# Kernel tuning notes

Measured on AMD Instinct MI355X. Metric: run time of the kernel, lower is better.

Reference implementation:

```python
import jax, jax.numpy as jnp
import numpy as np

B, L, D, K = 8, 1024, 1024, 128
VOCAB, N_ATOM_FEAT, N_TIMESTEPS = 160, 512, 1000
NEG = jnp.finfo(jnp.float32).min
SCALING = K ** (-0.5)


def setup_inputs() -> dict:
    key = jax.random.key(0)
    ks = jax.random.split(key, 14)
    inp = {}
    # forward args
    inp["token_id"] = jax.random.randint(ks[0], (B, L), 0, VOCAB)  # 0 => padding
    inp["node_attr"] = jax.random.randint(ks[1], (B, L, 9), 0, N_ATOM_FEAT)
    inp["is_molecule"] = jax.random.randint(ks[2], (B,), 0, 2).astype(bool)
    inp["pos"] = jax.random.normal(ks[3], (B, L, 3), jnp.float32) * 10.0
    inp["time_step"] = jax.random.randint(ks[4], (B, L), 0, N_TIMESTEPS)
    # learned parameters
    inp["embed_table"] = jax.random.normal(ks[5], (VOCAB, D), jnp.float32) * 0.02
    inp["atom_feat_table"] = jax.random.normal(ks[6], (N_ATOM_FEAT, D), jnp.float32) * 0.02
    inp["time_table"] = jax.random.normal(ks[7], (N_TIMESTEPS, D), jnp.float32) * 0.02
    inp["time_w1"] = jax.random.normal(ks[8], (D, D), jnp.float32) * (D ** -0.5)
    inp["time_b1"] = jnp.zeros((D,), jnp.float32)
    inp["time_w2"] = jax.random.normal(ks[9], (D, D), jnp.float32) * (D ** -0.5)
    inp["time_b2"] = jnp.zeros((D,), jnp.float32)
    inp["pos_emb_w"] = jax.random.normal(ks[10], (1, K), jnp.float32)          # Linear(1 -> K), no bias
    inp["pos_feature_w"] = jax.random.normal(ks[11], (K, D), jnp.float32) * (K ** -0.5)  # Linear(K -> D), no bias
    return inp


def _pos_emb(pos, padding_mask, pos_emb_w, pos_feature_w):
    # pos: [B,L,3], padding_mask: [B,L] bool
    delta = pos[:, :, None, :] - pos[:, None, :, :]          # [B,L,L,3]
    dist = 1.0 / (jnp.linalg.norm(delta, axis=-1) + 1.0)     # [B,L,L]
    # masked_fill on key side (expand_mask) and query side (padding_mask)
    mask = padding_mask[:, None, :] | padding_mask[:, :, None]
    dist = jnp.where(mask, NEG, dist)
    # value projection: Linear(1->K) on per-atom radial norm, zeroed at padding
    pe = jnp.linalg.norm(pos, axis=-1, keepdims=True) @ pos_emb_w  # [B,L,K]
    pe = jnp.where(padding_mask[:, :, None], 0.0, pe)
    attn = jax.nn.softmax(dist * SCALING, axis=-1)            # [B,L,L]
    pfe = jnp.einsum("bqk,bkc->bqc", attn, pe)                 # [B,L,K]
    pfe = pfe @ pos_feature_w                                  # [B,L,D]
    return jnp.where(padding_mask[:, :, None], 0.0, pfe)


def reference(token_id, node_attr, is_molecule, pos, time_step,
              embed_table, atom_feat_table, time_table,
              time_w1, time_b1, time_w2, time_b2,
              pos_emb_w, pos_feature_w):
    padding_mask = token_id == 0                               # [B,L]
    x = embed_table[token_id]                                  # [B,L,D]
    # 2D atom features: embed cols 1: and sum over feature axis
    atom_emb = atom_feat_table[node_attr[:, :, 1:]].sum(axis=-2)  # [B,L,D]
    atom_emb = jnp.where(is_molecule[:, None, None], atom_emb, 0.0)
    x = x + atom_emb
    # time step encoder: learnable embedding + Linear-SiLU-Linear MLP
    t = time_table[time_step]                                   # [B,L,D]
    time_embed = jax.nn.silu(t @ time_w1 + time_b1) @ time_w2 + time_b2
    x = x + time_embed
    # pairwise 3D positional embedding (softmax attention over 1/(r+1))
    x = x + _pos_emb(pos, padding_mask, pos_emb_w, pos_feature_w)
    return x, padding_mask
```

## Files before the change

kernel.cpp:

```cpp
#include <hip/hip_runtime.h>
#include <hip/hip_bf16.h>
#include <math.h>

#define BB 8
#define LL 1024
#define DD 1024
#define KK 128
#define NTS 1000
#define VOCAB 160
#define NATOM 512
#define SCALE 0.08838834764831845f

typedef __attribute__((ext_vector_type(8))) short short8;
typedef __attribute__((ext_vector_type(4))) float f32x4;

__device__ __forceinline__ unsigned short f2bf(float x) {
    __hip_bfloat16 h = __float2bfloat16(x);
    return *reinterpret_cast<unsigned short*>(&h);
}
__device__ __forceinline__ float bf2f(unsigned short u) {
    return __uint_as_float(((unsigned int)u) << 16);
}

__global__ __launch_bounds__(256) void prep_kernel(
    const float* __restrict__ w1,
    const float* __restrict__ w2,
    const float* __restrict__ embed_f,
    const float* __restrict__ atom_f,
    const float* __restrict__ pos_emb_w,
    const float* __restrict__ pos_feature_w,
    const void*  __restrict__ is_mol_raw,
    unsigned short* __restrict__ W1t,
    unsigned short* __restrict__ W2t,
    unsigned short* __restrict__ embed_bf,
    unsigned short* __restrict__ atom_bf,
    float* __restrict__ v,
    int*   __restrict__ is_mol_out)
{
    __shared__ float tile[32][33];
    const int blk = blockIdx.x;

    if (blk < 2048) {
        const int which = blk >> 10;
        const int idx = blk & 1023;
        const float* in = which ? w2 : w1;
        unsigned short* out = which ? W2t : W1t;
        const int bx = (idx & 31) * 32, by = (idx >> 5) * 32;
        const int tx = threadIdx.x & 31, ty = threadIdx.x >> 5;
        #pragma unroll
        for (int r = 0; r < 32; r += 8)
            tile[ty + r][tx] = in[(size_t)(by + ty + r) * DD + bx + tx];
        __syncthreads();
        #pragma unroll
        for (int r = 0; r < 32; r += 8)
            out[(size_t)(bx + ty + r) * DD + by + tx] = f2bf(tile[tx][ty + r]);
    } else if (blk < 2208) {
        const int e = ((blk - 2048) * 256 + threadIdx.x) * 4;
        float4 vv = *(const float4*)&embed_f[e];
        ushort4 o = { f2bf(vv.x), f2bf(vv.y), f2bf(vv.z), f2bf(vv.w) };
        *(ushort4*)&embed_bf[e] = o;
    } else if (blk < 2720) {
        const int e = ((blk - 2208) * 256 + threadIdx.x) * 4;
        float4 vv = *(const float4*)&atom_f[e];
        ushort4 o = { f2bf(vv.x), f2bf(vv.y), f2bf(vv.z), f2bf(vv.w) };
        *(ushort4*)&atom_bf[e] = o;
    } else if (blk < 2724) {
        int d = (blk - 2720) * 256 + threadIdx.x;
        float acc = 0.0f;
        #pragma unroll 4
        for (int c = 0; c < KK; ++c)
            acc += pos_emb_w[c] * pos_feature_w[c * DD + d];
        v[d] = acc;
    } else {
        if (threadIdx.x == 0) {
            const int* ip = (const int*)is_mol_raw;
            const unsigned char* cp = (const unsigned char*)is_mol_raw;
            bool all_bin = true;
            for (int i = 0; i < BB; ++i) {
                int x = ip[i];
                if (x != 0 && x != 1) all_bin = false;
            }
            for (int i = 0; i < BB; ++i)
                is_mol_out[i] = all_bin ? (ip[i] != 0) : (cp[i] != 0);
        }
    }
}

template <int MODE>
__global__ __launch_bounds__(256) void mfma_gemm32(
    const void* __restrict__ Ap,
    const unsigned short* __restrict__ Bt,
    const float* __restrict__ bias,
    unsigned short* __restrict__ Cout)
{
    __shared__ __align__(16) unsigned short As[32][136];
    __shared__ __align__(16) unsigned short Bs[32][136];

    const int tid  = threadIdx.x;
    const int lane = tid & 63;
    const int wave = tid >> 6;
    const int wm = wave >> 1, wn = wave & 1;
    const int quad = lane >> 4, l16 = lane & 15;
    const int mBase = blockIdx.y * 32, nBase = blockIdx.x * 32;

    f32x4 acc = {0.f, 0.f, 0.f, 0.f};

    const int r0 = tid >> 4, ko = (tid & 15) * 8;
    const int rowB0 = nBase + r0,      rowB1 = nBase + r0 + 16;
    int rowA0 = mBase + r0,            rowA1 = mBase + r0 + 16;
    if (MODE == 0) {
        if (rowA0 >= NTS) rowA0 = NTS - 1;
        if (rowA1 >= NTS) rowA1 = NTS - 1;
    }

    for (int k0 = 0; k0 < DD; k0 += 128) {
        if (MODE == 0) {
            const float* A = (const float*)Ap;
            float4 a00 = *(const float4*)&A[(size_t)rowA0 * DD + k0 + ko];
            float4 a01 = *(const float4*)&A[(size_t)rowA0 * DD + k0 + ko + 4];
            float4 a10 = *(const float4*)&A[(size_t)rowA1 * DD + k0 + ko];
            float4 a11 = *(const float4*)&A[(size_t)rowA1 * DD + k0 + ko + 4];
            short8 s0, s1;
            s0[0]=f2bf(a00.x); s0[1]=f2bf(a00.y); s0[2]=f2bf(a00.z); s0[3]=f2bf(a00.w);
            s0[4]=f2bf(a01.x); s0[5]=f2bf(a01.y); s0[6]=f2bf(a01.z); s0[7]=f2bf(a01.w);
            s1[0]=f2bf(a10.x); s1[1]=f2bf(a10.y); s1[2]=f2bf(a10.z); s1[3]=f2bf(a10.w);
            s1[4]=f2bf(a11.x); s1[5]=f2bf(a11.y); s1[6]=f2bf(a11.z); s1[7]=f2bf(a11.w);
            *(short8*)&As[r0][ko]      = s0;
            *(short8*)&As[r0 + 16][ko] = s1;
        } else {
            const unsigned short* A = (const unsigned short*)Ap;
            float4 a0 = *(const float4*)&A[(size_t)rowA0 * DD + k0 + ko];
            float4 a1 = *(const float4*)&A[(size_t)rowA1 * DD + k0 + ko];
            *(float4*)&As[r0][ko]      = a0;
            *(float4*)&As[r0 + 16][ko] = a1;
        }
        float4 b0 = *(const float4*)&Bt[(size_t)rowB0 * DD + k0 + ko];
        float4 b1 = *(const float4*)&Bt[(size_t)rowB1 * DD + k0 + ko];
        *(float4*)&Bs[r0][ko]      = b0;
        *(float4*)&Bs[r0 + 16][ko] = b1;
        __syncthreads();

        #pragma unroll
        for (int kk = 0; kk < 128; kk += 32) {
            short8 af = *(const short8*)&As[wm * 16 + l16][kk + quad * 8];
            short8 bf = *(const short8*)&Bs[wn * 16 + l16][kk + quad * 8];
            acc = __builtin_amdgcn_mfma_f32_16x16x32_bf16(af, bf, acc, 0, 0, 0);
        }
        __syncthreads();
    }

    const int col = nBase + wn * 16 + l16;
    const float bv = bias[col];
    #pragma unroll
    for (int r4 = 0; r4 < 4; ++r4) {
        const int row = mBase + wm * 16 + quad * 4 + r4;
        float val = acc[r4] + bv;
        if (MODE == 0) val = val / (1.0f + __expf(-val));
        Cout[(size_t)row * DD + col] = f2bf(val);
    }
}

__global__ __launch_bounds__(256) void fused_all(
    const int*   __restrict__ token_id,
    const int*   __restrict__ node_attr,
    const float* __restrict__ pos,
    const int*   __restrict__ time_step,
    const unsigned short* __restrict__ embed_bf,
    const unsigned short* __restrict__ atom_bf,
    const unsigned short* __restrict__ Ebf,
    const float* __restrict__ v,
    const int*   __restrict__ is_mol,
    float* __restrict__ out)
{
    __shared__ float4 keys[LL];
    __shared__ float  sS[8];

    const int blk   = blockIdx.x;
    const int batch = blk >> 7;
    const int q0    = (blk & 127) << 3;
    const int tid   = threadIdx.x;
    const int lane  = tid & 63, wave = tid >> 6;

    #pragma unroll
    for (int i = 0; i < 4; ++i) {
        const int k = tid + i * 256;
        const int t = batch * LL + k;
        const float x = pos[t * 3 + 0];
        const float y = pos[t * 3 + 1];
        const float z = pos[t * 3 + 2];
        const int tok = token_id[t];
        const float n = sqrtf(x * x + y * y + z * z);
        keys[k] = make_float4(x, y, z, tok == 0 ? -1.0f : n);
    }
    __syncthreads();

    #pragma unroll
    for (int qi = 0; qi < 2; ++qi) {
        const int ql = wave * 2 + qi;
        const float4 qk = keys[q0 + ql];
        float lsum = 0.0f, lws = 0.0f;
        #pragma unroll 4
        for (int i = 0; i < 16; ++i) {
            const float4 kd = keys[lane + i * 64];
            const float dx = qk.x - kd.x, dy = qk.y - kd.y, dz = qk.z - kd.z;
            const float dn = sqrtf(dx * dx + dy * dy + dz * dz);
            const float e = __expf(SCALE / (dn + 1.0f));
            const bool valid = kd.w >= 0.0f;
            const float ev = valid ? e : 0.0f;
            lsum += ev;
            lws  += ev * (valid ? kd.w : 0.0f);
        }
        #pragma unroll
        for (int off = 32; off > 0; off >>= 1) {
            lsum += __shfl_xor(lsum, off);
            lws  += __shfl_xor(lws,  off);
        }
        if (lane == 0)
            sS[ql] = (qk.w < 0.0f) ? 0.0f : (lws / lsum);
    }
    __syncthreads();

    const int im   = is_mol[batch];
    const int half = tid >> 7;
    const int tl   = tid & 127;
    const int j    = tl * 8;
    const float4 v0 = *(const float4*)&v[j];
    const float4 v1 = *(const float4*)&v[j + 4];

    #pragma unroll
    for (int qp = 0; qp < 4; ++qp) {
        const int ql  = qp * 2 + half;
        const int t   = batch * LL + q0 + ql;
        const int tok = token_id[t];
        const int ts  = time_step[t];
        const float s = sS[ql];

        float o[8];
        short8 eb = *(const short8*)&embed_bf[(size_t)tok * DD + j];
        #pragma unroll
        for (int d = 0; d < 8; ++d) o[d] = bf2f((unsigned short)eb[d]);

        if (im) {
            #pragma unroll
            for (int f = 1; f < 9; ++f) {
                const int a = node_attr[t * 9 + f];
                short8 ab = *(const short8*)&atom_bf[(size_t)a * DD + j];
                #pragma unroll
                for (int d = 0; d < 8; ++d) o[d] += bf2f((unsigned short)ab[d]);
            }
        }
        short8 er = *(const short8*)&Ebf[(size_t)ts * DD + j];
        #pragma unroll
        for (int d = 0; d < 8; ++d) o[d] += bf2f((unsigned short)er[d]);

        o[0] += s * v0.x; o[1] += s * v0.y; o[2] += s * v0.z; o[3] += s * v0.w;
        o[4] += s * v1.x; o[5] += s * v1.y; o[6] += s * v1.z; o[7] += s * v1.w;

        float4 w0 = {o[0], o[1], o[2], o[3]};
        float4 w1 = {o[4], o[5], o[6], o[7]};
        *(float4*)&out[(size_t)t * DD + j]     = w0;
        *(float4*)&out[(size_t)t * DD + j + 4] = w1;
    }

    if (tid < 8) {
        const int t = batch * LL + q0 + tid;
        out[(size_t)BB * LL * DD + t] = (keys[q0 + tid].w < 0.0f) ? 1.0f : 0.0f;
    }
}

extern "C" void kernel_launch(void* const* d_in, const int* in_sizes, int n_in,
                              void* d_out, int out_size, void* d_ws, size_t ws_size,
                              hipStream_t stream)
{
    const int*   token_id      = (const int*)  d_in[0];
    const int*   node_attr     = (const int*)  d_in[1];
    const void*  is_mol_raw    = (const void*) d_in[2];
    const float* pos           = (const float*)d_in[3];
    const int*   time_step     = (const int*)  d_in[4];
    const float* embed_table   = (const float*)d_in[5];
    const float* atom_feat     = (const float*)d_in[6];
    const float* time_table    = (const float*)d_in[7];
    const float* w1            = (const float*)d_in[8];
    const float* b1            = (const float*)d_in[9];
    const float* w2            = (const float*)d_in[10];
    const float* b2            = (const float*)d_in[11];
    const float* pos_emb_w     = (const float*)d_in[12];
    const float* pos_feature_w = (const float*)d_in[13];

    float* out = (float*)d_out;
    char*  ws  = (char*)d_ws;

    unsigned short* W1t      = (unsigned short*)(ws);
    unsigned short* Ebf      = (unsigned short*)(ws);
    unsigned short* H        = (unsigned short*)(ws + (2u << 20));
    unsigned short* W2t      = (unsigned short*)(ws + (4u << 20));
    unsigned short* embed_bf = (unsigned short*)(ws + (6u << 20));
    unsigned short* atom_bf  = (unsigned short*)(ws + (6u << 20) + (512u << 10));
    float*          V        = (float*)(ws + (7u << 20) + (512u << 10));
    int*            is_mol_r = (int*)(V + 1024);

    prep_kernel<<<2725, 256, 0, stream>>>(w1, w2, embed_table, atom_feat,
                                          pos_emb_w, pos_feature_w, is_mol_raw,
                                          W1t, W2t, embed_bf, atom_bf,
                                          V, is_mol_r);

    dim3 g(32, 32);
    mfma_gemm32<0><<<g, 256, 0, stream>>>((const void*)time_table, W1t, b1, H);
    mfma_gemm32<1><<<g, 256, 0, stream>>>((const void*)H,          W2t, b2, Ebf);

    fused_all<<<1024, 256, 0, stream>>>(token_id, node_attr, pos, time_step,
                                        embed_bf, atom_bf, Ebf, V,
                                        is_mol_r, out);
}
```

Baseline: 149.4 us.

## Rebalance kernel stages so independent prep and softmax work overlaps the first GEMM

The launch sequence is restructured. Only the W1 transpose runs first. The first time-MLP GEMM then runs in one grid together with the W2 transpose, the table conversions, the v vector, the is_molecule decode and the pairwise softmax reduction, which writes per-query scalars to workspace. The final assemble kernel now only gathers embeddings and adds s*v. This removes the softmax from the critical path after the second GEMM and fills idle CUs during the small GEMM. The cost is a heterogeneous grid with a larger shared-memory union and an extra global round trip for the scalars.

```diff
diff --git a/kernel.cpp b/kernel.cpp
--- a/kernel.cpp
+++ b/kernel.cpp
@@ -7,8 +7,6 @@
 #define DD 1024
 #define KK 128
 #define NTS 1000
-#define VOCAB 160
-#define NATOM 512
 #define SCALE 0.08838834764831845f
 
 typedef __attribute__((ext_vector_type(8))) short short8;
@@ -22,57 +20,149 @@
     return __uint_as_float(((unsigned int)u) << 16);
 }
 
-__global__ __launch_bounds__(256) void prep_kernel(
-    const float* __restrict__ w1,
+union SMem {
+    struct { unsigned short As[32][136]; unsigned short Bs[32][136]; } g;
+    float4 keys[LL];
+    float  tile[32][33];
+};
+
+__device__ __forceinline__ void transpose_tile(
+    const float* __restrict__ in, unsigned short* __restrict__ out,
+    int idx, SMem& sm)
+{
+    const int tid = threadIdx.x;
+    const int bx = (idx & 31) * 32, by = (idx >> 5) * 32;
+    const int tx = tid & 31, ty = tid >> 5;
+    #pragma unroll
+    for (int r = 0; r < 32; r += 8)
+        sm.tile[ty + r][tx] = in[(size_t)(by + ty + r) * DD + bx + tx];
+    __syncthreads();
+    #pragma unroll
+    for (int r = 0; r < 32; r += 8)
+        out[(size_t)(bx + ty + r) * DD + by + tx] = f2bf(sm.tile[tx][ty + r]);
+}
+
+__device__ __forceinline__ void gemm32_tile(
+    const float* __restrict__ Af, const unsigned short* __restrict__ Ab,
+    const unsigned short* __restrict__ Bt, const float* __restrict__ bias,
+    unsigned short* __restrict__ Cout, int mBase, int nBase, int do_silu,
+    SMem& sm)
+{
+    const int tid  = threadIdx.x;
+    const int lane = tid & 63, wave = tid >> 6;
+    const int wm = wave >> 1, wn = wave & 1;
+    const int quad = lane >> 4, l16 = lane & 15;
+
+    f32x4 acc = {0.f, 0.f, 0.f, 0.f};
+
+    const int r0 = tid >> 4, ko = (tid & 15) * 8;
+    const int rowB0 = nBase + r0, rowB1 = nBase + r0 + 16;
+    int rowA0 = mBase + r0, rowA1 = mBase + r0 + 16;
+    if (Af) {
+        if (rowA0 >= NTS) rowA0 = NTS - 1;
+        if (rowA1 >= NTS) rowA1 = NTS - 1;
+    }
+
+    for (int k0 = 0; k0 < DD; k0 += 128) {
+        if (Af) {
+            float4 a00 = *(const float4*)&Af[(size_t)rowA0 * DD + k0 + ko];
+            float4 a01 = *(const float4*)&Af[(size_t)rowA0 * DD + k0 + ko + 4];
+            float4 a10 = *(const float4*)&Af[(size_t)rowA1 * DD + k0 + ko];
+            float4 a11 = *(const float4*)&Af[(size_t)rowA1 * DD + k0 + ko + 4];
+            short8 s0, s1;
+            s0[0]=f2bf(a00.x); s0[1]=f2bf(a00.y); s0[2]=f2bf(a00.z); s0[3]=f2bf(a00.w);
+            s0[4]=f2bf(a01.x); s0[5]=f2bf(a01.y); s0[6]=f2bf(a01.z); s0[7]=f2bf(a01.w);
+            s1[0]=f2bf(a10.x); s1[1]=f2bf(a10.y); s1[2]=f2bf(a10.z); s1[3]=f2bf(a10.w);
+            s1[4]=f2bf(a11.x); s1[5]=f2bf(a11.y); s1[6]=f2bf(a11.z); s1[7]=f2bf(a11.w);
+            *(short8*)&sm.g.As[r0][ko]      = s0;
+            *(short8*)&sm.g.As[r0 + 16][ko] = s1;
+        } else {
+            float4 a0 = *(const float4*)&Ab[(size_t)rowA0 * DD + k0 + ko];
+            float4 a1 = *(const float4*)&Ab[(size_t)rowA1 * DD + k0 + ko];
+            *(float4*)&sm.g.As[r0][ko]      = a0;
+            *(float4*)&sm.g.As[r0 + 16][ko] = a1;
+        }
+        float4 b0 = *(const float4*)&Bt[(size_t)rowB0 * DD + k0 + ko];
+        float4 b1 = *(const float4*)&Bt[(size_t)rowB1 * DD + k0 + ko];
+        *(float4*)&sm.g.Bs[r0][ko]      = b0;
+        *(float4*)&sm.g.Bs[r0 + 16][ko] = b1;
+        __syncthreads();
+
+        #pragma unroll
+        for (int kk = 0; kk < 128; kk += 32) {
+            short8 af = *(const short8*)&sm.g.As[wm * 16 + l16][kk + quad * 8];
+            short8 bf = *(const short8*)&sm.g.Bs[wn * 16 + l16][kk + quad * 8];
+            acc = __builtin_amdgcn_mfma_f32_16x16x32_bf16(af, bf, acc, 0, 0, 0);
+        }
+        __syncthreads();
+    }
+
+    const int col = nBase + wn * 16 + l16;
+    const float bv = bias[col];
+    #pragma unroll
+    for (int r4 = 0; r4 < 4; ++r4) {
+        const int row = mBase + wm * 16 + quad * 4 + r4;
+        float val = acc[r4] + bv;
+        if (do_silu) val = val / (1.0f + __expf(-val));
+        Cout[(size_t)row * DD + col] = f2bf(val);
+    }
+}
+
+__global__ __launch_bounds__(256) void prep1(
+    const float* __restrict__ w1, unsigned short* __restrict__ W1t)
+{
+    __shared__ SMem sm;
+    transpose_tile(w1, W1t, blockIdx.x, sm);
+}
+
+__global__ __launch_bounds__(256) void mid(
+    const float* __restrict__ time_table,
+    const unsigned short* __restrict__ W1t,
+    const float* __restrict__ b1,
     const float* __restrict__ w2,
     const float* __restrict__ embed_f,
     const float* __restrict__ atom_f,
     const float* __restrict__ pos_emb_w,
     const float* __restrict__ pos_feature_w,
     const void*  __restrict__ is_mol_raw,
-    unsigned short* __restrict__ W1t,
+    const int*   __restrict__ token_id,
+    const float* __restrict__ pos,
+    unsigned short* __restrict__ H,
     unsigned short* __restrict__ W2t,
     unsigned short* __restrict__ embed_bf,
     unsigned short* __restrict__ atom_bf,
     float* __restrict__ v,
-    int*   __restrict__ is_mol_out)
-{
-    __shared__ float tile[32][33];
+    int*   __restrict__ is_mol_out,
+    float* __restrict__ sSg)
+{
+    __shared__ SMem sm;
     const int blk = blockIdx.x;
-
-    if (blk < 2048) {
-        const int which = blk >> 10;
-        const int idx = blk & 1023;
-        const float* in = which ? w2 : w1;
-        unsigned short* out = which ? W2t : W1t;
-        const int bx = (idx & 31) * 32, by = (idx >> 5) * 32;
-        const int tx = threadIdx.x & 31, ty = threadIdx.x >> 5;
-        #pragma unroll
-        for (int r = 0; r < 32; r += 8)
-            tile[ty + r][tx] = in[(size_t)(by + ty + r) * DD + bx + tx];
-        __syncthreads();
-        #pragma unroll
-        for (int r = 0; r < 32; r += 8)
-            out[(size_t)(bx + ty + r) * DD + by + tx] = f2bf(tile[tx][ty + r]);
+    const int tid = threadIdx.x;
+
+    if (blk < 1024) {
+        gemm32_tile(time_table, nullptr, W1t, b1, H,
+                    (blk >> 5) * 32, (blk & 31) * 32, 1, sm);
+    } else if (blk < 2048) {
+        transpose_tile(w2, W2t, blk - 1024, sm);
     } else if (blk < 2208) {
-        const int e = ((blk - 2048) * 256 + threadIdx.x) * 4;
+        const int e = ((blk - 2048) * 256 + tid) * 4;
         float4 vv = *(const float4*)&embed_f[e];
         ushort4 o = { f2bf(vv.x), f2bf(vv.y), f2bf(vv.z), f2bf(vv.w) };
         *(ushort4*)&embed_bf[e] = o;
     } else if (blk < 2720) {
-        const int e = ((blk - 2208) * 256 + threadIdx.x) * 4;
+        const int e = ((blk - 2208) * 256 + tid) * 4;
         float4 vv = *(const float4*)&atom_f[e];
         ushort4 o = { f2bf(vv.x), f2bf(vv.y), f2bf(vv.z), f2bf(vv.w) };
         *(ushort4*)&atom_bf[e] = o;
     } else if (blk < 2724) {
-        int d = (blk - 2720) * 256 + threadIdx.x;
+        const int d = (blk - 2720) * 256 + tid;
         float acc = 0.0f;
         #pragma unroll 4
         for (int c = 0; c < KK; ++c)
             acc += pos_emb_w[c] * pos_feature_w[c * DD + d];
         v[d] = acc;
-    } else {
-        if (threadIdx.x == 0) {
+    } else if (blk == 2724) {
+        if (tid == 0) {
             const int* ip = (const int*)is_mol_raw;
             const unsigned char* cp = (const unsigned char*)is_mol_raw;
             bool all_bin = true;
@@ -83,142 +173,79 @@
             for (int i = 0; i < BB; ++i)
                 is_mol_out[i] = all_bin ? (ip[i] != 0) : (cp[i] != 0);
         }
-    }
-}
-
-template <int MODE>
-__global__ __launch_bounds__(256) void mfma_gemm32(
-    const void* __restrict__ Ap,
-    const unsigned short* __restrict__ Bt,
-    const float* __restrict__ bias,
-    unsigned short* __restrict__ Cout)
-{
-    __shared__ __align__(16) unsigned short As[32][136];
-    __shared__ __align__(16) unsigned short Bs[32][136];
-
-    const int tid  = threadIdx.x;
-    const int lane = tid & 63;
-    const int wave = tid >> 6;
-    const int wm = wave >> 1, wn = wave & 1;
-    const int quad = lane >> 4, l16 = lane & 15;
-    const int mBase = blockIdx.y * 32, nBase = blockIdx.x * 32;
-
-    f32x4 acc = {0.f, 0.f, 0.f, 0.f};
-
-    const int r0 = tid >> 4, ko = (tid & 15) * 8;
-    const int rowB0 = nBase + r0,      rowB1 = nBase + r0 + 16;
-    int rowA0 = mBase + r0,            rowA1 = mBase + r0 + 16;
-    if (MODE == 0) {
-        if (rowA0 >= NTS) rowA0 = NTS - 1;
-        if (rowA1 >= NTS) rowA1 = NTS - 1;
-    }
-
-    for (int k0 = 0; k0 < DD; k0 += 128) {
-        if (MODE == 0) {
-            const float* A = (const float*)Ap;
-            float4 a00 = *(const float4*)&A[(size_t)rowA0 * DD + k0 + ko];
-            float4 a01 = *(const float4*)&A[(size_t)rowA0 * DD + k0 + ko + 4];
-            float4 a10 = *(const float4*)&A[(size_t)rowA1 * DD + k0 + ko];
-            float4 a11 = *(const float4*)&A[(size_t)rowA1 * DD + k0 + ko + 4];
-            short8 s0, s1;
-            s0[0]=f2bf(a00.x); s0[1]=f2bf(a00.y); s0[2]=f2bf(a00.z); s0[3]=f2bf(a00.w);
-            s0[4]=f2bf(a01.x); s0[5]=f2bf(a01.y); s0[6]=f2bf(a01.z); s0[7]=f2bf(a01.w);
-            s1[0]=f2bf(a10.x); s1[1]=f2bf(a10.y); s1[2]=f2bf(a10.z); s1[3]=f2bf(a10.w);
-            s1[4]=f2bf(a11.x); s1[5]=f2bf(a11.y); s1[6]=f2bf(a11.z); s1[7]=f2bf(a11.w);
-            *(short8*)&As[r0][ko]      = s0;
-            *(short8*)&As[r0 + 16][ko] = s1;
-        } else {
-            const unsigned short* A = (const unsigned short*)Ap;
-            float4 a0 = *(const float4*)&A[(size_t)rowA0 * DD + k0 + ko];
-            float4 a1 = *(const float4*)&A[(size_t)rowA1 * DD + k0 + ko];
-            *(float4*)&As[r0][ko]      = a0;
-            *(float4*)&As[r0 + 16][ko] = a1;
-        }
-        float4 b0 = *(const float4*)&Bt[(size_t)rowB0 * DD + k0 + ko];
-        float4 b1 = *(const float4*)&Bt[(size_t)rowB1 * DD + k0 + ko];
-        *(float4*)&Bs[r0][ko]      = b0;
-        *(float4*)&Bs[r0 + 16][ko] = b1;
+    } else {
+        const int ab = blk - 2725;
+        const int batch = ab >> 6;
+        const int q0 = (ab & 63) * 16;
+        const int lane = tid & 63, wave = tid >> 6;
+
+        #pragma unroll
+        for (int i = 0; i < 4; ++i) {
+            const int k = tid + i * 256;
+            const int t = batch * LL + k;
+            const float x = pos[t * 3 + 0];
+            const float y = pos[t * 3 + 1];
+            const float z = pos[t * 3 + 2];
+            const int tok = token_id[t];
+            const float n = sqrtf(x * x + y * y + z * z);
+            sm.keys[k] = make_float4(x, y, z, tok == 0 ? -1.0f : n);
+        }
         __syncthreads();
 
         #pragma unroll
-        for (int kk = 0; kk < 128; kk += 32) {
-            short8 af = *(const short8*)&As[wm * 16 + l16][kk + quad * 8];
-            short8 bf = *(const short8*)&Bs[wn * 16 + l16][kk + quad * 8];
-            acc = __builtin_amdgcn_mfma_f32_16x16x32_bf16(af, bf, acc, 0, 0, 0);
-        }
-        __syncthreads();
-    }
-
-    const int col = nBase + wn * 16 + l16;
-    const float bv = bias[col];
-    #pragma unroll
-    for (int r4 = 0; r4 < 4; ++r4) {
-        const int row = mBase + wm * 16 + quad * 4 + r4;
-        float val = acc[r4] + bv;
-        if (MODE == 0) val = val / (1.0f + __expf(-val));
-        Cout[(size_t)row * DD + col] = f2bf(val);
-    }
-}
-
-__global__ __launch_bounds__(256) void fused_all(
+        for (int qi = 0; qi < 4; ++qi) {
+            const int ql = wave * 4 + qi;
+            const float4 qk = sm.keys[q0 + ql];
+            float lsum = 0.0f, lws = 0.0f;
+            #pragma unroll 4
+            for (int i = 0; i < 16; ++i) {
+                const float4 kd = sm.keys[lane + i * 64];
+                const float dx = qk.x - kd.x, dy = qk.y - kd.y, dz = qk.z - kd.z;
+                const float dn = sqrtf(dx * dx + dy * dy + dz * dz);
+                const float e = __expf(SCALE / (dn + 1.0f));
+                const bool valid = kd.w >= 0.0f;
+                const float ev = valid ? e : 0.0f;
+                lsum += ev;
+                lws  += ev * (valid ? kd.w : 0.0f);
+            }
+            #pragma unroll
+            for (int off = 32; off > 0; off >>= 1) {
+                lsum += __shfl_xor(lsum, off);
+                lws  += __shfl_xor(lws,  off);
+            }
+            if (lane == 0)
+                sSg[batch * LL + q0 + ql] = (qk.w < 0.0f) ? 0.0f : (lws / lsum);
+        }
+    }
+}
+
+__global__ __launch_bounds__(256) void gemm2k(
+    const unsigned short* __restrict__ H,
+    const unsigned short* __restrict__ W2t,
+    const float* __restrict__ b2,
+    unsigned short* __restrict__ Ebf)
+{
+    __shared__ SMem sm;
+    gemm32_tile(nullptr, H, W2t, b2, Ebf,
+                (blockIdx.x >> 5) * 32, (blockIdx.x & 31) * 32, 0, sm);
+}
+
+__global__ __launch_bounds__(256) void assemble(
     const int*   __restrict__ token_id,
     const int*   __restrict__ node_attr,
-    const float* __restrict__ pos,
     const int*   __restrict__ time_step,
     const unsigned short* __restrict__ embed_bf,
     const unsigned short* __restrict__ atom_bf,
     const unsigned short* __restrict__ Ebf,
     const float* __restrict__ v,
+    const float* __restrict__ sSg,
     const int*   __restrict__ is_mol,
     float* __restrict__ out)
 {
-    __shared__ float4 keys[LL];
-    __shared__ float  sS[8];
-
     const int blk   = blockIdx.x;
     const int batch = blk >> 7;
     const int q0    = (blk & 127) << 3;
     const int tid   = threadIdx.x;
-    const int lane  = tid & 63, wave = tid >> 6;
-
-    #pragma unroll
-    for (int i = 0; i < 4; ++i) {
-        const int k = tid + i * 256;
-        const int t = batch * LL + k;
-        const float x = pos[t * 3 + 0];
-        const float y = pos[t * 3 + 1];
-        const float z = pos[t * 3 + 2];
-        const int tok = token_id[t];
-        const float n = sqrtf(x * x + y * y + z * z);
-        keys[k] = make_float4(x, y, z, tok == 0 ? -1.0f : n);
-    }
-    __syncthreads();
-
-    #pragma unroll
-    for (int qi = 0; qi < 2; ++qi) {
-        const int ql = wave * 2 + qi;
-        const float4 qk = keys[q0 + ql];
-        float lsum = 0.0f, lws = 0.0f;
-        #pragma unroll 4
-        for (int i = 0; i < 16; ++i) {
-            const float4 kd = keys[lane + i * 64];
-            const float dx = qk.x - kd.x, dy = qk.y - kd.y, dz = qk.z - kd.z;
-            const float dn = sqrtf(dx * dx + dy * dy + dz * dz);
-            const float e = __expf(SCALE / (dn + 1.0f));
-            const bool valid = kd.w >= 0.0f;
-            const float ev = valid ? e : 0.0f;
-            lsum += ev;
-            lws  += ev * (valid ? kd.w : 0.0f);
-        }
-        #pragma unroll
-        for (int off = 32; off > 0; off >>= 1) {
-            lsum += __shfl_xor(lsum, off);
-            lws  += __shfl_xor(lws,  off);
-        }
-        if (lane == 0)
-            sS[ql] = (qk.w < 0.0f) ? 0.0f : (lws / lsum);
-    }
-    __syncthreads();
 
     const int im   = is_mol[batch];
     const int half = tid >> 7;
@@ -233,7 +260,7 @@
         const int t   = batch * LL + q0 + ql;
         const int tok = token_id[t];
         const int ts  = time_step[t];
-        const float s = sS[ql];
+        const float s = sSg[t];
 
         float o[8];
         short8 eb = *(const short8*)&embed_bf[(size_t)tok * DD + j];
@@ -256,15 +283,15 @@
         o[0] += s * v0.x; o[1] += s * v0.y; o[2] += s * v0.z; o[3] += s * v0.w;
         o[4] += s * v1.x; o[5] += s * v1.y; o[6] += s * v1.z; o[7] += s * v1.w;
 
-        float4 w0 = {o[0], o[1], o[2], o[3]};
-        float4 w1 = {o[4], o[5], o[6], o[7]};
-        *(float4*)&out[(size_t)t * DD + j]     = w0;
-        *(float4*)&out[(size_t)t * DD + j + 4] = w1;
+        float4 wlo = {o[0], o[1], o[2], o[3]};
+        float4 whi = {o[4], o[5], o[6], o[7]};
+        *(float4*)&out[(size_t)t * DD + j]     = wlo;
+        *(float4*)&out[(size_t)t * DD + j + 4] = whi;
     }
 
     if (tid < 8) {
         const int t = batch * LL + q0 + tid;
-        out[(size_t)BB * LL * DD + t] = (keys[q0 + tid].w < 0.0f) ? 1.0f : 0.0f;
+        out[(size_t)BB * LL * DD + t] = (token_id[t] == 0) ? 1.0f : 0.0f;
     }
 }
 
@@ -296,19 +323,21 @@
     unsigned short* W2t      = (unsigned short*)(ws + (4u << 20));
     unsigned short* embed_bf = (unsigned short*)(ws + (6u << 20));
     unsigned short* atom_bf  = (unsigned short*)(ws + (6u << 20) + (512u << 10));
-    float*          V        = (float*)(ws + (7u << 20) + (512u << 10));
-    int*            is_mol_r = (int*)(V + 1024);
-
-    prep_kernel<<<2725, 256, 0, stream>>>(w1, w2, embed_table, atom_feat,
-                                          pos_emb_w, pos_feature_w, is_mol_raw,
-                                          W1t, W2t, embed_bf, atom_bf,
-                                          V, is_mol_r);
-
-    dim3 g(32, 32);
-    mfma_gemm32<0><<<g, 256, 0, stream>>>((const void*)time_table, W1t, b1, H);
-    mfma_gemm32<1><<<g, 256, 0, stream>>>((const void*)H,          W2t, b2, Ebf);
-
-    fused_all<<<1024, 256, 0, stream>>>(token_id, node_attr, pos, time_step,
-                                        embed_bf, atom_bf, Ebf, V,
-                                        is_mol_r, out);
-}
+    char*           base7    = ws + (7u << 20) + (512u << 10);
+    float*          V        = (float*)(base7);
+    float*          sSg      = (float*)(base7 + (4u << 10));
+    int*            is_mol_r = (int*)  (base7 + (36u << 10));
+
+    prep1<<<1024, 256, 0, stream>>>(w1, W1t);
+
+    mid<<<3237, 256, 0, stream>>>(time_table, W1t, b1, w2, embed_table,
+                                  atom_feat, pos_emb_w, pos_feature_w,
+                                  is_mol_raw, token_id, pos,
+                                  H, W2t, embed_bf, atom_bf, V, is_mol_r, sSg);
+
+    gemm2k<<<1024, 256, 0, stream>>>(H, W2t, b2, Ebf);
+
+    assemble<<<1024, 256, 0, stream>>>(token_id, node_attr, time_step,
+                                       embed_bf, atom_bf, Ebf, V, sSg,
+                                       is_mol_r, out);
+}
```

Result: faster. 144.8 us (-3.1%).
